# Kernel tuning notes

Measured on AMD Instinct MI355X. Metric: run time of the kernel, lower is better.

Reference implementation:

```python
import jax, jax.numpy as jnp
import numpy as np
from jax import lax

BITW = 1
BITA = 3


def _ste_round(x, n):
    # round with straight-through gradient (Round -> Identity override)
    return x + lax.stop_gradient(jnp.round(x * n) / n - x)


def _quantize_active(x, bitA):
    # cabs: clip |x| to [0, 1], then k-bit uniform quantization with STE round
    x = jnp.minimum(1.0, jnp.abs(x))
    if bitA == 32:
        return x
    n = float(2 ** bitA - 1)
    return _ste_round(x, n)


def _quantize_weight(w, bitW):
    if bitW == 32:
        return w
    if bitW == 1:
        # sign with STE (Sign -> Identity): grad w.r.t. w is 1
        E = lax.stop_gradient(jnp.mean(jnp.abs(w)))
        y = w / E
        return (y + lax.stop_gradient(jnp.sign(y) - y)) * E
    n = float(2 ** bitW - 1)
    w = jnp.clip(w * 0.5 + 0.5, 0.0, 1.0)
    return 2.0 * _ste_round(w, n) - 1.0


def setup_inputs() -> dict:
    key = jax.random.key(0)
    kx, kw, kb = jax.random.split(key, 3)
    x = jax.random.normal(kx, (32, 56, 56, 256), dtype=jnp.float32)
    W = jax.random.normal(kw, (3, 3, 256, 256), dtype=jnp.float32) * 0.02  # HWIO
    b = jax.random.normal(kb, (256,), dtype=jnp.float32) * 0.01
    return {"x": x, "W": W, "b": b}


def reference(x, W, b):
    xq = _quantize_active(x, BITA)          # [N,H,W,C] quantized activations
    wq = _quantize_weight(W, BITW)          # [kh,kw,Cin,Cout] binarized weights
    out = lax.conv_general_dilated(
        xq, wq,
        window_strides=(1, 1),
        padding="SAME",
        dimension_numbers=("NHWC", "HWIO", "NHWC"),
    )
    return out + b  # act = identity
```

## Files before the change

kernel.cpp:

```cpp
#include <hip/hip_runtime.h>

typedef __attribute__((ext_vector_type(4))) int int4v;
typedef __attribute__((ext_vector_type(16))) int int16v;

#define NPIX 100352
#define KTAP 2304
#define LDK 144

__global__ __launch_bounds__(256) void quant_w_kernel(const float* __restrict__ Wm,
                                                      signed char* __restrict__ Bt,
                                                      float* __restrict__ Esum) {
  int j4 = blockIdx.x * 256 + threadIdx.x;
  int byte0 = j4 * 4;
  int cout = byte0 / KTAP;
  int k0 = byte0 - cout * KTAP;
  float s = 0.f;
  unsigned int packed = 0;
#pragma unroll
  for (int i = 0; i < 4; ++i) {
    float w = Wm[(k0 + i) * 256 + cout];
    s += fabsf(w);
    int sg = (w > 0.f) ? 1 : ((w < 0.f) ? -1 : 0);
    packed |= ((unsigned int)(sg & 0xFF)) << (8 * i);
  }
  ((unsigned int*)Bt)[j4] = packed;
#pragma unroll
  for (int o = 32; o > 0; o >>= 1) s += __shfl_down(s, o, 64);
  if ((threadIdx.x & 63) == 0) atomicAdd(Esum, s);
}

__global__ __launch_bounds__(256) void quant_x_kernel(const float* __restrict__ x,
                                                      signed char* __restrict__ xq) {
  int t = blockIdx.x * 256 + threadIdx.x;
  float4 v = ((const float4*)x)[t];
  unsigned int q = 0;
  q |= (unsigned int)(int)rintf(fminf(1.f, fabsf(v.x)) * 7.f);
  q |= ((unsigned int)(int)rintf(fminf(1.f, fabsf(v.y)) * 7.f)) << 8;
  q |= ((unsigned int)(int)rintf(fminf(1.f, fabsf(v.z)) * 7.f)) << 16;
  q |= ((unsigned int)(int)rintf(fminf(1.f, fabsf(v.w)) * 7.f)) << 24;
  ((unsigned int*)xq)[t] = q;
}

__global__ __launch_bounds__(256) void conv_kernel(const signed char* __restrict__ xq,
                                                   const signed char* __restrict__ Bt,
                                                   const float* __restrict__ bias,
                                                   const float* __restrict__ Esum,
                                                   float* __restrict__ out) {
  __shared__ signed char As[128 * LDK];
  __shared__ signed char Bs[128 * LDK];

  const int t = threadIdx.x;
  const int lane = t & 63;
  const int m0 = blockIdx.x * 128;
  const int n0 = blockIdx.y * 128;
  const int wid = t >> 6;
  const int wm = (wid & 1) * 64;
  const int wn = (wid >> 1) * 64;

  const int rbase = t >> 3;
  const int colb = (t & 7) * 16;

  int pix[4], hh[4], ww[4];
#pragma unroll
  for (int i = 0; i < 4; ++i) {
    int p = m0 + rbase + 32 * i;
    pix[i] = p;
    int rem = p % 3136;
    hh[i] = rem / 56;
    ww[i] = rem % 56;
  }

  int16v acc[2][2];
#pragma unroll
  for (int a = 0; a < 2; ++a)
#pragma unroll
    for (int b = 0; b < 2; ++b)
#pragma unroll
      for (int r = 0; r < 16; ++r) acc[a][b][r] = 0;

  const int lrow = lane & 31;
  const int khalf = (lane >> 5) * 16;

  for (int tap = 0; tap < 9; ++tap) {
    const int dh = tap / 3 - 1;
    const int dw = tap % 3 - 1;
#pragma unroll
    for (int half = 0; half < 2; ++half) {
      const int kofs = tap * 256 + half * 128;
      const int cofs = half * 128;
      __syncthreads();
#pragma unroll
      for (int i = 0; i < 4; ++i) {
        const int r = rbase + 32 * i;
        int4v a = {0, 0, 0, 0};
        if ((unsigned)(hh[i] + dh) < 56u && (unsigned)(ww[i] + dw) < 56u) {
          a = *(const int4v*)(xq + (long)(pix[i] + dh * 56 + dw) * 256 + cofs + colb);
        }
        *(int4v*)(As + r * LDK + colb) = a;
      }
#pragma unroll
      for (int i = 0; i < 4; ++i) {
        const int r = rbase + 32 * i;
        int4v b = *(const int4v*)(Bt + (long)(n0 + r) * KTAP + kofs + colb);
        *(int4v*)(Bs + r * LDK + colb) = b;
      }
      __syncthreads();
#pragma unroll
      for (int ks = 0; ks < 4; ++ks) {
        const int ko = ks * 32 + khalf;
        int4v a0 = *(const int4v*)(As + (wm + lrow) * LDK + ko);
        int4v a1 = *(const int4v*)(As + (wm + 32 + lrow) * LDK + ko);
        int4v b0 = *(const int4v*)(Bs + (wn + lrow) * LDK + ko);
        int4v b1 = *(const int4v*)(Bs + (wn + 32 + lrow) * LDK + ko);
        acc[0][0] = __builtin_amdgcn_mfma_i32_32x32x32_i8(a0, b0, acc[0][0], 0, 0, 0);
        acc[0][1] = __builtin_amdgcn_mfma_i32_32x32x32_i8(a0, b1, acc[0][1], 0, 0, 0);
        acc[1][0] = __builtin_amdgcn_mfma_i32_32x32x32_i8(a1, b0, acc[1][0], 0, 0, 0);
        acc[1][1] = __builtin_amdgcn_mfma_i32_32x32x32_i8(a1, b1, acc[1][1], 0, 0, 0);
      }
    }
  }

  const float scale = Esum[0] * (1.0f / (589824.0f * 7.0f));
#pragma unroll
  for (int mt = 0; mt < 2; ++mt)
#pragma unroll
    for (int nt = 0; nt < 2; ++nt) {
      const int col = n0 + wn + nt * 32 + lrow;
      const float bv = bias[col];
#pragma unroll
      for (int r = 0; r < 16; ++r) {
        const int row = (r & 3) + 8 * (r >> 2) + 4 * (lane >> 5);
        const int m = m0 + wm + mt * 32 + row;
        out[(long)m * 256 + col] = (float)acc[mt][nt][r] * scale + bv;
      }
    }
}

extern "C" void kernel_launch(void* const* d_in, const int* in_sizes, int n_in,
                              void* d_out, int out_size, void* d_ws, size_t ws_size,
                              hipStream_t stream) {
  const float* x    = (const float*)d_in[0];
  const float* Wm   = (const float*)d_in[1];
  const float* bias = (const float*)d_in[2];
  float* out = (float*)d_out;

  float* Esum = (float*)d_ws;
  signed char* Bt = (signed char*)d_ws + 256;
  signed char* xq = (signed char*)d_ws + 256 + 589824;

  hipMemsetAsync(d_ws, 0, 4, stream);
  quant_w_kernel<<<576, 256, 0, stream>>>(Wm, Bt, Esum);
  quant_x_kernel<<<25088, 256, 0, stream>>>(x, xq);
  conv_kernel<<<dim3(784, 2), 256, 0, stream>>>(xq, Bt, bias, Esum, out);
}
```

Measured before the change: 297.6 us.

## Widen conv tile to full Cout, add register prefetch, transpose weights via LDS

The conv kernel now computes all 256 output channels per block (128x256 tile, 8 accumulators per wave), so each activation tile is loaded once instead of twice. A register-staged prefetch of the next K-slice overlaps global loads with MFMA work, and per-tap boundary masks are precomputed. The weight quantization kernel is rewritten to read coalesced rows and transpose through shared memory. The larger tile raises register and LDS use, which may limit occupancy.

```diff
diff --git a/kernel.cpp b/kernel.cpp
--- a/kernel.cpp
+++ b/kernel.cpp
@@ -10,23 +10,30 @@
 __global__ __launch_bounds__(256) void quant_w_kernel(const float* __restrict__ Wm,
                                                       signed char* __restrict__ Bt,
                                                       float* __restrict__ Esum) {
-  int j4 = blockIdx.x * 256 + threadIdx.x;
-  int byte0 = j4 * 4;
-  int cout = byte0 / KTAP;
-  int k0 = byte0 - cout * KTAP;
+  __shared__ signed char sT[64][80];
+  __shared__ float red[4];
+  const int k0 = blockIdx.x * 64;
+  const int c0 = blockIdx.y * 64;
+  const int t = threadIdx.x;
+  const int cc = t & 63;
+  const int r0 = (t >> 6) * 16;
   float s = 0.f;
-  unsigned int packed = 0;
 #pragma unroll
-  for (int i = 0; i < 4; ++i) {
-    float w = Wm[(k0 + i) * 256 + cout];
+  for (int i = 0; i < 16; ++i) {
+    const int k = r0 + i;
+    float w = Wm[(long)(k0 + k) * 256 + c0 + cc];
     s += fabsf(w);
-    int sg = (w > 0.f) ? 1 : ((w < 0.f) ? -1 : 0);
-    packed |= ((unsigned int)(sg & 0xFF)) << (8 * i);
+    sT[cc][k] = (signed char)((w > 0.f) ? 1 : ((w < 0.f) ? -1 : 0));
   }
-  ((unsigned int*)Bt)[j4] = packed;
 #pragma unroll
   for (int o = 32; o > 0; o >>= 1) s += __shfl_down(s, o, 64);
-  if ((threadIdx.x & 63) == 0) atomicAdd(Esum, s);
+  if ((t & 63) == 0) red[t >> 6] = s;
+  __syncthreads();
+  if (t == 0) atomicAdd(Esum, red[0] + red[1] + red[2] + red[3]);
+  const int co = t >> 2;
+  const int kc = (t & 3) * 16;
+  int4v v = *(const int4v*)&sT[co][kc];
+  *(int4v*)(Bt + (long)(c0 + co) * KTAP + k0 + kc) = v;
 }
 
 __global__ __launch_bounds__(256) void quant_x_kernel(const float* __restrict__ x,
@@ -41,82 +48,100 @@
   ((unsigned int*)xq)[t] = q;
 }
 
-__global__ __launch_bounds__(256) void conv_kernel(const signed char* __restrict__ xq,
-                                                   const signed char* __restrict__ Bt,
-                                                   const float* __restrict__ bias,
-                                                   const float* __restrict__ Esum,
-                                                   float* __restrict__ out) {
+__global__ __launch_bounds__(256, 2) void conv_kernel(const signed char* __restrict__ xq,
+                                                      const signed char* __restrict__ Bt,
+                                                      const float* __restrict__ bias,
+                                                      const float* __restrict__ Esum,
+                                                      float* __restrict__ out) {
   __shared__ signed char As[128 * LDK];
-  __shared__ signed char Bs[128 * LDK];
+  __shared__ signed char Bs[256 * LDK];
 
   const int t = threadIdx.x;
   const int lane = t & 63;
+  const int wid = t >> 6;
   const int m0 = blockIdx.x * 128;
-  const int n0 = blockIdx.y * 128;
-  const int wid = t >> 6;
   const int wm = (wid & 1) * 64;
-  const int wn = (wid >> 1) * 64;
+  const int wn = (wid >> 1) * 128;
 
   const int rbase = t >> 3;
   const int colb = (t & 7) * 16;
 
-  int pix[4], hh[4], ww[4];
+  int abase[4];
+  unsigned avalid[4];
 #pragma unroll
   for (int i = 0; i < 4; ++i) {
-    int p = m0 + rbase + 32 * i;
-    pix[i] = p;
-    int rem = p % 3136;
-    hh[i] = rem / 56;
-    ww[i] = rem % 56;
+    const int p = m0 + rbase + 32 * i;
+    const int rem = p % 3136;
+    const int h = rem / 56, w = rem % 56;
+    abase[i] = p * 256 + colb;
+    unsigned mask = 0;
+#pragma unroll
+    for (int tap = 0; tap < 9; ++tap) {
+      const int dh = tap / 3 - 1, dw = tap % 3 - 1;
+      if ((unsigned)(h + dh) < 56u && (unsigned)(w + dw) < 56u) mask |= 1u << tap;
+    }
+    avalid[i] = mask;
   }
+  int bofs[8];
+#pragma unroll
+  for (int i = 0; i < 8; ++i) bofs[i] = (rbase + 32 * i) * KTAP + colb;
 
-  int16v acc[2][2];
+  int16v acc[2][4];
 #pragma unroll
   for (int a = 0; a < 2; ++a)
 #pragma unroll
-    for (int b = 0; b < 2; ++b)
+    for (int b = 0; b < 4; ++b)
 #pragma unroll
       for (int r = 0; r < 16; ++r) acc[a][b][r] = 0;
 
+  int4v ra[4], rb[8];
+
+  auto prefetch = [&](int s) {
+    const int tap = s >> 1, hf = s & 1;
+    const int dh = tap / 3 - 1, dw = tap % 3 - 1;
+    const int shift = (dh * 56 + dw) * 256 + hf * 128;
+    const int kofs = tap * 256 + hf * 128;
+#pragma unroll
+    for (int i = 0; i < 4; ++i) {
+      int4v a = {0, 0, 0, 0};
+      if (avalid[i] & (1u << tap)) a = *(const int4v*)(xq + (long)(abase[i] + shift));
+      ra[i] = a;
+    }
+#pragma unroll
+    for (int i = 0; i < 8; ++i) rb[i] = *(const int4v*)(Bt + (long)(bofs[i] + kofs));
+  };
+
+  prefetch(0);
   const int lrow = lane & 31;
   const int khalf = (lane >> 5) * 16;
 
-  for (int tap = 0; tap < 9; ++tap) {
-    const int dh = tap / 3 - 1;
-    const int dw = tap % 3 - 1;
+  for (int s = 0; s < 18; ++s) {
+    if (s) __syncthreads();
 #pragma unroll
-    for (int half = 0; half < 2; ++half) {
-      const int kofs = tap * 256 + half * 128;
-      const int cofs = half * 128;
-      __syncthreads();
+    for (int i = 0; i < 4; ++i)
+      *(int4v*)(As + (rbase + 32 * i) * LDK + colb) = ra[i];
 #pragma unroll
-      for (int i = 0; i < 4; ++i) {
-        const int r = rbase + 32 * i;
-        int4v a = {0, 0, 0, 0};
-        if ((unsigned)(hh[i] + dh) < 56u && (unsigned)(ww[i] + dw) < 56u) {
-          a = *(const int4v*)(xq + (long)(pix[i] + dh * 56 + dw) * 256 + cofs + colb);
-        }
-        *(int4v*)(As + r * LDK + colb) = a;
-      }
+    for (int i = 0; i < 8; ++i)
+      *(int4v*)(Bs + (rbase + 32 * i) * LDK + colb) = rb[i];
+    __syncthreads();
+    if (s + 1 < 18) prefetch(s + 1);
 #pragma unroll
-      for (int i = 0; i < 4; ++i) {
-        const int r = rbase + 32 * i;
-        int4v b = *(const int4v*)(Bt + (long)(n0 + r) * KTAP + kofs + colb);
-        *(int4v*)(Bs + r * LDK + colb) = b;
-      }
-      __syncthreads();
-#pragma unroll
-      for (int ks = 0; ks < 4; ++ks) {
-        const int ko = ks * 32 + khalf;
-        int4v a0 = *(const int4v*)(As + (wm + lrow) * LDK + ko);
-        int4v a1 = *(const int4v*)(As + (wm + 32 + lrow) * LDK + ko);
-        int4v b0 = *(const int4v*)(Bs + (wn + lrow) * LDK + ko);
-        int4v b1 = *(const int4v*)(Bs + (wn + 32 + lrow) * LDK + ko);
-        acc[0][0] = __builtin_amdgcn_mfma_i32_32x32x32_i8(a0, b0, acc[0][0], 0, 0, 0);
-        acc[0][1] = __builtin_amdgcn_mfma_i32_32x32x32_i8(a0, b1, acc[0][1], 0, 0, 0);
-        acc[1][0] = __builtin_amdgcn_mfma_i32_32x32x32_i8(a1, b0, acc[1][0], 0, 0, 0);
-        acc[1][1] = __builtin_amdgcn_mfma_i32_32x32x32_i8(a1, b1, acc[1][1], 0, 0, 0);
-      }
+    for (int ks = 0; ks < 4; ++ks) {
+      const int ko = ks * 32 + khalf;
+      int4v a0 = *(const int4v*)(As + (wm + lrow) * LDK + ko);
+      int4v a1 = *(const int4v*)(As + (wm + 32 + lrow) * LDK + ko);
+      int4v b0 = *(const int4v*)(Bs + (wn + lrow) * LDK + ko);
+      int4v b1 = *(const int4v*)(Bs + (wn + 32 + lrow) * LDK + ko);
+      int4v b2 = *(const int4v*)(Bs + (wn + 64 + lrow) * LDK + ko);
+      int4v b3 = *(const int4v*)(Bs + (wn + 96 + lrow) * LDK + ko);
+      acc[0][0] = __builtin_amdgcn_mfma_i32_32x32x32_i8(a0, b0, acc[0][0], 0, 0, 0);
+      acc[0][1] = __builtin_amdgcn_mfma_i32_32x32x32_i8(a0, b1, acc[0][1], 0, 0, 0);
+      acc[0][2] = __builtin_amdgcn_mfma_i32_32x32x32_i8(a0, b2, acc[0][2], 0, 0, 0);
+      acc[0][3] = __builtin_amdgcn_mfma_i32_32x32x32_i8(a0, b3, acc[0][3], 0, 0, 0);
+      acc[1][0] = __builtin_amdgcn_mfma_i32_32x32x32_i8(a1, b0, acc[1][0], 0, 0, 0);
+      acc[1][1] = __builtin_amdgcn_mfma_i32_32x32x32_i8(a1, b1, acc[1][1], 0, 0, 0);
+      acc[1][2] = __builtin_amdgcn_mfma_i32_32x32x32_i8(a1, b2, acc[1][2], 0, 0, 0);
+      acc[1][3] = __builtin_amdgcn_mfma_i32_32x32x32_i8(a1, b3, acc[1][3], 0, 0, 0);
     }
   }
 
@@ -124,8 +149,8 @@
 #pragma unroll
   for (int mt = 0; mt < 2; ++mt)
 #pragma unroll
-    for (int nt = 0; nt < 2; ++nt) {
-      const int col = n0 + wn + nt * 32 + lrow;
+    for (int nt = 0; nt < 4; ++nt) {
+      const int col = wn + nt * 32 + lrow;
       const float bv = bias[col];
 #pragma unroll
       for (int r = 0; r < 16; ++r) {
@@ -149,7 +174,7 @@
   signed char* xq = (signed char*)d_ws + 256 + 589824;
 
   hipMemsetAsync(d_ws, 0, 4, stream);
-  quant_w_kernel<<<576, 256, 0, stream>>>(Wm, Bt, Esum);
+  quant_w_kernel<<<dim3(36, 4), 256, 0, stream>>>(Wm, Bt, Esum);
   quant_x_kernel<<<25088, 256, 0, stream>>>(x, xq);
-  conv_kernel<<<dim3(784, 2), 256, 0, stream>>>(xq, Bt, bias, Esum, out);
+  conv_kernel<<<784, 256, 0, stream>>>(xq, Bt, bias, Esum, out);
 }
```

Measured after the change: 249.2 us. 16.3% less time.
